# Kernel optimization log

Measured on AMD Instinct MI355X. Metric: run time of the kernel, lower is better.

Reference implementation:

```python
import jax, jax.numpy as jnp
import numpy as np

N_NODES = 50000
N_EDGES = 1_600_000
N_GRAPHS = 64
EMB = 1280
GCN_DIMS = [128, 256, 256]
FC_DIMS = [1024, 128]
EPS = 1e-5  # BatchNorm eps (torch default)


def setup_inputs() -> dict:
    key = jax.random.key(0)
    ks = jax.random.split(key, 16)
    inp = {}
    inp["x"] = jax.random.normal(ks[0], (N_NODES, EMB), jnp.float32)
    inp["edge_index"] = jax.random.randint(ks[1], (2, N_EDGES), 0, N_NODES)
    inp["batch"] = jnp.sort(jax.random.randint(ks[2], (N_NODES,), 0, N_GRAPHS))
    dims = [EMB] + GCN_DIMS
    for i in range(3):
        inp[f"Wg{i}"] = jax.random.normal(ks[3 + i], (dims[i], dims[i + 1]), jnp.float32) * (1.0 / np.sqrt(dims[i]))
        inp[f"bg{i}"] = jnp.zeros((dims[i + 1],), jnp.float32)
        inp[f"gamma{i}"] = jnp.ones((dims[i + 1],), jnp.float32)
        inp[f"beta{i}"] = jnp.zeros((dims[i + 1],), jnp.float32)
    fdims = [GCN_DIMS[-1]] + FC_DIMS
    for i in range(2):
        inp[f"Wf{i}"] = jax.random.normal(ks[10 + i], (fdims[i], fdims[i + 1]), jnp.float32) * (1.0 / np.sqrt(fdims[i]))
        inp[f"bf{i}"] = jnp.zeros((fdims[i + 1],), jnp.float32)
    return inp


def _batchnorm(h, gamma, beta):
    # training-mode BN over node dim, biased variance (torch normalization)
    m = h.mean(axis=0)
    v = h.var(axis=0)
    return gamma * (h - m) * jax.lax.rsqrt(v + EPS) + beta


def reference(x, edge_index, batch,
              Wg0, bg0, gamma0, beta0,
              Wg1, bg1, gamma1, beta1,
              Wg2, bg2, gamma2, beta2,
              Wf0, bf0, Wf1, bf1):
    # --- GCN symmetric normalization with self-loops (PyG GCNConv default) ---
    loop = jnp.arange(N_NODES)
    src = jnp.concatenate([edge_index[0], loop])  # message sources
    dst = jnp.concatenate([edge_index[1], loop])  # aggregation targets
    deg = jax.ops.segment_sum(jnp.ones(src.shape[0], jnp.float32), dst, num_segments=N_NODES)
    dinv = jnp.where(deg > 0, jax.lax.rsqrt(jnp.maximum(deg, 1.0)), 0.0)
    norm = dinv[src] * dinv[dst]  # [E + N]

    def gcn_conv(h, W, b):
        h = h @ W                               # [N, d_out] transform first (PyG order)
        msg = h[src] * norm[:, None]            # gather + scale
        return jax.ops.segment_sum(msg, dst, num_segments=N_NODES) + b

    h = x
    for W, b, g, bt in ((Wg0, bg0, gamma0, beta0),
                        (Wg1, bg1, gamma1, beta1),
                        (Wg2, bg2, gamma2, beta2)):
        h = gcn_conv(h, W, b)
        h = _batchnorm(h, g, bt)
        h = jax.nn.relu(h)
        # dropout is identity in eval mode

    # --- global mean pool over graphs ---
    counts = jax.ops.segment_sum(jnp.ones(N_NODES, jnp.float32), batch, num_segments=N_GRAPHS)
    sums = jax.ops.segment_sum(h, batch, num_segments=N_GRAPHS)
    g = sums / jnp.maximum(counts, 1.0)[:, None]  # [B, 256]

    # --- FC head ---
    g = jax.nn.relu(g @ Wf0 + bf0)
    out = g @ Wf1 + bf1                           # [B, 128]
    return out
```

## Files before the change

kernel.cpp:

```cpp
#include <hip/hip_runtime.h>
#include <hip/hip_bf16.h>

#define N_NODES 50000
#define N_EDGES 1600000
#define N_GRAPHS 64
#define MT_TILES 1563

typedef _Float16 f16;
typedef _Float16 f16x8 __attribute__((ext_vector_type(8)));
typedef _Float16 f16x4 __attribute__((ext_vector_type(4)));
typedef _Float16 f16x2 __attribute__((ext_vector_type(2)));
typedef float f32x4 __attribute__((ext_vector_type(4)));

template <int V> struct VecT;
template <> struct VecT<2> { using type = f16x2; };
template <> struct VecT<4> { using type = f16x4; };

__global__ void init_deg(int* deg) {
    int i = blockIdx.x * blockDim.x + threadIdx.x;
    if (i < N_NODES) deg[i] = 1;
}

__global__ void deg_count(const int* __restrict__ dst, int* __restrict__ deg) {
    int e = blockIdx.x * blockDim.x + threadIdx.x;
    if (e < N_EDGES) atomicAdd(&deg[dst[e]], 1);
}

__global__ void make_dinv(const int* __restrict__ deg, float* __restrict__ dinv) {
    int i = blockIdx.x * blockDim.x + threadIdx.x;
    if (i < N_NODES) dinv[i] = rsqrtf((float)deg[i]);
}

__global__ void scan_deg(const int* __restrict__ deg, int* __restrict__ rowstart,
                         int* __restrict__ pos) {
    __shared__ int wsum[16];
    __shared__ int carry_s;
    const int t = threadIdx.x;
    const int lane = t & 63;
    const int w = t >> 6;
    if (t == 0) carry_s = 0;
    __syncthreads();
    for (int base = 0; base < N_NODES; base += 1024) {
        int i = base + t;
        int v = (i < N_NODES) ? (deg[i] - 1) : 0;
        int s = v;
#pragma unroll
        for (int off = 1; off < 64; off <<= 1) {
            int n = __shfl_up(s, off, 64);
            if (lane >= off) s += n;
        }
        if (lane == 63) wsum[w] = s;
        __syncthreads();
        if (w == 0) {
            int ws = (lane < 16) ? wsum[lane] : 0;
#pragma unroll
            for (int off = 1; off < 16; off <<= 1) {
                int n = __shfl_up(ws, off, 64);
                if (lane >= off) ws += n;
            }
            if (lane < 16) wsum[lane] = ws;
        }
        __syncthreads();
        int waveoff = (w == 0) ? 0 : wsum[w - 1];
        int carry = carry_s;
        int excl = carry + waveoff + s - v;
        if (i < N_NODES) {
            rowstart[i] = excl;
            pos[i] = excl;
        }
        __syncthreads();
        if (t == 0) carry_s = carry + wsum[15];
        __syncthreads();
    }
    if (t == 0) rowstart[N_NODES] = carry_s;
}

__global__ void csr_fill(const int* __restrict__ src, const int* __restrict__ dst,
                         const float* __restrict__ dinv, int* __restrict__ pos,
                         int2* __restrict__ csr) {
    int e = blockIdx.x * blockDim.x + threadIdx.x;
    if (e >= N_EDGES) return;
    int s = src[e], d = dst[e];
    int slot = atomicAdd(&pos[d], 1);
    csr[slot] = make_int2(s, __float_as_int(dinv[s] * dinv[d]));
}

__global__ void cast_w(const float* __restrict__ W, f16* __restrict__ Wt, int K, int N) {
    int i = blockIdx.x * blockDim.x + threadIdx.x;
    if (i >= K * N) return;
    int k = i % K, n = i / K;
    Wt[i] = (f16)W[(size_t)k * N + n];
}

__launch_bounds__(256)
__global__ void cast_x_blocked(const float* __restrict__ x, f16* __restrict__ xb) {
    const int mt = blockIdx.x;
    const int t = threadIdx.x;
    const size_t base = (size_t)mt * 32 * 1280;
    const size_t tbase = (size_t)mt * 40 * 1024;
#pragma unroll 4
    for (int i = 0; i < 40; ++i) {
        int f = i * 1024 + t * 4;
        int r = f / 1280;
        int k = f - r * 1280;
        float4 v = make_float4(0.f, 0.f, 0.f, 0.f);
        if (mt * 32 + r < N_NODES) v = *(const float4*)(x + base + f);
        int kt = k >> 5, kk = k & 31;
        f16x4 o = {(f16)v.x, (f16)v.y, (f16)v.z, (f16)v.w};
        *(f16x4*)(xb + tbase + (size_t)kt * 1024 + r * 32 + kk) = o;
    }
}

__launch_bounds__(256)
__global__ void gemm_xb_f16_sk(const f16* __restrict__ xb, const f16* __restrict__ Bt,
                               float* __restrict__ C0, float* __restrict__ C1) {
    const int K = 1280;
    const int gw = (int)((blockIdx.x * blockDim.x + threadIdx.x) >> 6);
    if (gw >= 6250) return;
    const int lane = threadIdx.x & 63;
    const int m16 = gw >> 1, s = gw & 1;
    const int mt = m16 >> 1, half = m16 & 1;
    float* __restrict__ C = s ? C1 : C0;
    const int r = lane & 15, q = lane >> 4;
    const f16* at = xb + (size_t)mt * 40960 + (size_t)s * 20480 + half * 512 + r * 32 + q * 8;
    const f16* bp = Bt + (size_t)r * K + s * 640 + q * 8;

    f32x4 acc[8];
#pragma unroll
    for (int j = 0; j < 8; ++j) acc[j] = (f32x4){0.f, 0.f, 0.f, 0.f};

#pragma unroll 4
    for (int kt = 0; kt < 20; ++kt) {
        f16x8 a = *(const f16x8*)(at + kt * 1024);
#pragma unroll
        for (int ni = 0; ni < 8; ++ni) {
            f16x8 bf = *(const f16x8*)(bp + (size_t)ni * 16 * K + kt * 32);
            acc[ni] = __builtin_amdgcn_mfma_f32_16x16x32_f16(a, bf, acc[ni], 0, 0, 0);
        }
    }
#pragma unroll
    for (int j = 0; j < 4; ++j) {
        int row = m16 * 16 + q * 4 + j;
        float* cp = C + (size_t)row * 128 + r;
#pragma unroll
        for (int ni = 0; ni < 8; ++ni) cp[ni * 16] = acc[ni][j];
    }
}

__global__ void reduce_cast(const float* __restrict__ c0, const float* __restrict__ c1,
                            f16* __restrict__ o, int n4) {
    int i = blockIdx.x * blockDim.x + threadIdx.x;
    if (i >= n4) return;
    float4 a = ((const float4*)c0)[i];
    float4 b = ((const float4*)c1)[i];
    f16x4 r = {(f16)(a.x + b.x), (f16)(a.y + b.y), (f16)(a.z + b.z), (f16)(a.w + b.w)};
    ((f16x4*)o)[i] = r;
}

template <int K>
__launch_bounds__(256)
__global__ void gemm_h_bn_f16(const f16* __restrict__ A16, const float* __restrict__ ss,
                              const f16* __restrict__ Bt, f16* __restrict__ C16, int N) {
    const int gw = (int)((blockIdx.x * blockDim.x + threadIdx.x) >> 6);
    if (gw >= N_NODES / 16) return;
    const int lane = threadIdx.x & 63;
    const int m0 = gw * 16;
    const int col0 = blockIdx.y * 128;
    const int r = lane & 15, q = lane >> 4;
    const f16* a0 = A16 + (size_t)(m0 + r) * K + q * 8;
    const f16* bp = Bt + (size_t)(col0 + r) * K + q * 8;

    f32x4 acc[8];
#pragma unroll
    for (int j = 0; j < 8; ++j) acc[j] = (f32x4){0.f, 0.f, 0.f, 0.f};

#pragma unroll
    for (int k0 = 0; k0 < K; k0 += 32) {
        f16x8 raw = *(const f16x8*)(a0 + k0);
        const int kb = k0 + q * 8;
        f16x8 af;
#pragma unroll
        for (int j = 0; j < 8; ++j) {
            float v = (float)raw[j] * ss[kb + j] + ss[K + kb + j];
            af[j] = (f16)(v > 0.f ? v : 0.f);
        }
#pragma unroll
        for (int ni = 0; ni < 8; ++ni) {
            f16x8 bf = *(const f16x8*)(bp + (size_t)ni * 16 * K + k0);
            acc[ni] = __builtin_amdgcn_mfma_f32_16x16x32_f16(af, bf, acc[ni], 0, 0, 0);
        }
    }
#pragma unroll
    for (int j = 0; j < 4; ++j) {
        int row = m0 + q * 4 + j;
        f16* cp = C16 + (size_t)row * N + col0 + r;
#pragma unroll
        for (int ni = 0; ni < 8; ++ni) cp[ni * 16] = (f16)acc[ni][j];
    }
}

template <int D>
__launch_bounds__(256)
__global__ void aggregate(const f16* __restrict__ h, const int* __restrict__ rowstart,
                          const int2* __restrict__ csr, const float* __restrict__ dinv,
                          const float* __restrict__ bias, f16* __restrict__ out) {
    constexpr int V = D / 64;
    using vec = typename VecT<V>::type;
    int w = (int)((blockIdx.x * blockDim.x + threadIdx.x) >> 6);
    int lane = threadIdx.x & 63;
    if (w >= N_NODES) return;
    float acc[V];
    float di = dinv[w];
    vec self = *(const vec*)(h + (size_t)w * D + lane * V);
#pragma unroll
    for (int v = 0; v < V; ++v) acc[v] = (float)self[v] * (di * di);
    int e0 = rowstart[w], e1 = rowstart[w + 1];
    int j = e0;
    for (; j + 8 <= e1; j += 8) {
        int2 c[8];
        vec rr[8];
#pragma unroll
        for (int u = 0; u < 8; ++u) c[u] = csr[j + u];
#pragma unroll
        for (int u = 0; u < 8; ++u)
            rr[u] = *(const vec*)(h + (size_t)c[u].x * D + lane * V);
#pragma unroll
        for (int u = 0; u < 8; ++u) {
            float nm = __int_as_float(c[u].y);
#pragma unroll
            for (int v = 0; v < V; ++v) acc[v] += (float)rr[u][v] * nm;
        }
    }
    if (j + 4 <= e1) {
        int2 c0 = csr[j], c1 = csr[j + 1], c2 = csr[j + 2], c3 = csr[j + 3];
        vec r0 = *(const vec*)(h + (size_t)c0.x * D + lane * V);
        vec r1 = *(const vec*)(h + (size_t)c1.x * D + lane * V);
        vec r2 = *(const vec*)(h + (size_t)c2.x * D + lane * V);
        vec r3 = *(const vec*)(h + (size_t)c3.x * D + lane * V);
        float n0 = __int_as_float(c0.y), n1 = __int_as_float(c1.y);
        float n2 = __int_as_float(c2.y), n3 = __int_as_float(c3.y);
#pragma unroll
        for (int v = 0; v < V; ++v)
            acc[v] += (float)r0[v] * n0 + (float)r1[v] * n1 +
                      (float)r2[v] * n2 + (float)r3[v] * n3;
        j += 4;
    }
    for (; j < e1; ++j) {
        int2 c = csr[j];
        vec r = *(const vec*)(h + (size_t)c.x * D + lane * V);
        float nm = __int_as_float(c.y);
#pragma unroll
        for (int v = 0; v < V; ++v) acc[v] += (float)r[v] * nm;
    }
    vec o;
#pragma unroll
    for (int v = 0; v < V; ++v) o[v] = (f16)(acc[v] + bias[lane * V + v]);
    *(vec*)(out + (size_t)w * D + lane * V) = o;
}

template <int D>
__global__ void bn_stats(const f16* __restrict__ h, float* __restrict__ stat) {
    int f = threadIdx.x;
    int r0 = blockIdx.x * 128;
    int r1 = min(r0 + 128, N_NODES);
    float s = 0.f, s2 = 0.f;
    for (int r = r0; r < r1; ++r) {
        float v = (float)h[(size_t)r * D + f];
        s += v;
        s2 += v * v;
    }
    atomicAdd(&stat[f], s);
    atomicAdd(&stat[D + f], s2);
}

template <int D>
__global__ void bn_finalize(const float* __restrict__ stat, const float* __restrict__ gamma,
                            const float* __restrict__ beta, float* __restrict__ ss) {
    int f = threadIdx.x;
    float m = stat[f] * (1.0f / N_NODES);
    float var = stat[D + f] * (1.0f / N_NODES) - m * m;
    float sc = gamma[f] * rsqrtf(var + 1e-5f);
    ss[f] = sc;
    ss[D + f] = beta[f] - m * sc;
}

__global__ void count_batch_bs(const int* __restrict__ batch, int* __restrict__ cnt) {
    int g = threadIdx.x;
    if (g >= N_GRAPHS) return;
    int lo = 0, hi = N_NODES;
    while (lo < hi) { int mid = (lo + hi) >> 1; if (batch[mid] < g) lo = mid + 1; else hi = mid; }
    int b0 = lo;
    lo = 0; hi = N_NODES;
    while (lo < hi) { int mid = (lo + hi) >> 1; if (batch[mid] < g + 1) lo = mid + 1; else hi = mid; }
    cnt[g] = lo - b0;
}

__global__ void pool_seg_bn(const f16* __restrict__ h, const float* __restrict__ ss,
                            const int* __restrict__ batch, float* __restrict__ psum) {
    int f = threadIdx.x;
    float sc = ss[f], sh = ss[256 + f];
    int r0 = blockIdx.x * 64;
    int r1 = min(r0 + 64, N_NODES);
    float acc = 0.f;
    int cur = batch[r0];
    for (int r = r0; r < r1; ++r) {
        int b = batch[r];
        if (b != cur) {
            atomicAdd(&psum[cur * 256 + f], acc);
            acc = 0.f;
            cur = b;
        }
        float v = sc * (float)h[(size_t)r * 256 + f] + sh;
        acc += v > 0.f ? v : 0.f;
    }
    atomicAdd(&psum[cur * 256 + f], acc);
}

__global__ void pool_div(const float* __restrict__ psum, const int* __restrict__ cnt,
                         float* __restrict__ g) {
    int i = blockIdx.x * 256 + threadIdx.x;
    int b = i >> 8;
    float c = (float)max(cnt[b], 1);
    g[i] = psum[i] / c;
}

__global__ void fc_init(const float* __restrict__ b, float* __restrict__ Y, int rows, int N) {
    int i = blockIdx.x * blockDim.x + threadIdx.x;
    if (i < rows * N) Y[i] = b[i % N];
}

__global__ void fc_splitk(const float* __restrict__ X, const float* __restrict__ W,
                          float* __restrict__ Y, int K, int N, int KC) {
    int col = blockIdx.x * blockDim.x + threadIdx.x;
    int row = blockIdx.y;
    int k0 = blockIdx.z * KC;
    float acc = 0.f;
    const float* x = X + (size_t)row * K + k0;
    const float* w = W + (size_t)k0 * N + col;
#pragma unroll 8
    for (int k = 0; k < KC; ++k) acc += x[k] * w[(size_t)k * N];
    atomicAdd(&Y[(size_t)row * N + col], acc);
}

__global__ void relu_inplace(float* __restrict__ Y, int n) {
    int i = blockIdx.x * blockDim.x + threadIdx.x;
    if (i < n) Y[i] = Y[i] > 0.f ? Y[i] : 0.f;
}

extern "C" void kernel_launch(void* const* d_in, const int* in_sizes, int n_in,
                              void* d_out, int out_size, void* d_ws, size_t ws_size,
                              hipStream_t stream) {
    const float* x     = (const float*)d_in[0];
    const int*   ei    = (const int*)d_in[1];
    const int*   batch = (const int*)d_in[2];
    const float* Wg0 = (const float*)d_in[3],  *bg0 = (const float*)d_in[4];
    const float* gamma0 = (const float*)d_in[5], *beta0 = (const float*)d_in[6];
    const float* Wg1 = (const float*)d_in[7],  *bg1 = (const float*)d_in[8];
    const float* gamma1 = (const float*)d_in[9], *beta1 = (const float*)d_in[10];
    const float* Wg2 = (const float*)d_in[11], *bg2 = (const float*)d_in[12];
    const float* gamma2 = (const float*)d_in[13], *beta2 = (const float*)d_in[14];
    const float* Wf0 = (const float*)d_in[15], *bf0 = (const float*)d_in[16];
    const float* Wf1 = (const float*)d_in[17], *bf1 = (const float*)d_in[18];
    float* out = (float*)d_out;

    size_t off = 0;
    auto alloc = [&](size_t bytes) {
        void* p = (char*)d_ws + off;
        off += (bytes + 255) & ~(size_t)255;
        return p;
    };
    f16*   hA16     = (f16*)alloc((size_t)N_NODES * 256 * 2);
    float* cp32     = (float*)alloc((size_t)2 * N_NODES * 128 * 4);
    f16*   hBn16    = (f16*)cp32;
    float* cp0      = cp32;
    float* cp1      = cp32 + (size_t)N_NODES * 128;
    f16*   xb       = (f16*)alloc((size_t)MT_TILES * 40 * 1024 * 2);
    int2*  csr      = (int2*)alloc((size_t)N_EDGES * 8);
    int*   deg      = (int*)alloc((size_t)N_NODES * 4);
    float* dinv     = (float*)alloc((size_t)N_NODES * 4);
    int*   rowstart = (int*)alloc((size_t)(N_NODES + 1) * 4);
    int*   pos      = (int*)alloc((size_t)N_NODES * 4);
    float* bnstat   = (float*)alloc(2 * 256 * 4);
    float* bnss     = (float*)alloc(2 * 256 * 4);
    float* psum     = (float*)alloc(64 * 256 * 4);
    int*   pcount   = (int*)alloc(64 * 4);
    float* gpool    = (float*)alloc(64 * 256 * 4);
    float* g1       = (float*)alloc(64 * 1024 * 4);
    f16*   W0t      = (f16*)alloc((size_t)1280 * 128 * 2);
    f16*   W1t      = (f16*)alloc((size_t)128 * 256 * 2);
    f16*   W2t      = (f16*)alloc((size_t)256 * 256 * 2);
    (void)ws_size;

    const int TPB = 256;
    const int nb_nodes = (N_NODES + TPB - 1) / TPB;
    const int nb_edges = (N_EDGES + TPB - 1) / TPB;

    cast_x_blocked<<<MT_TILES, TPB, 0, stream>>>(x, xb);
    init_deg<<<nb_nodes, TPB, 0, stream>>>(deg);
    deg_count<<<nb_edges, TPB, 0, stream>>>(ei + N_EDGES, deg);
    make_dinv<<<nb_nodes, TPB, 0, stream>>>(deg, dinv);
    scan_deg<<<1, 1024, 0, stream>>>(deg, rowstart, pos);
    csr_fill<<<nb_edges, TPB, 0, stream>>>(ei, ei + N_EDGES, dinv, pos, csr);
    cast_w<<<(1280 * 128 + 255) / 256, 256, 0, stream>>>(Wg0, W0t, 1280, 128);
    cast_w<<<(128 * 256 + 255) / 256, 256, 0, stream>>>(Wg1, W1t, 128, 256);
    cast_w<<<(256 * 256 + 255) / 256, 256, 0, stream>>>(Wg2, W2t, 256, 256);

    const int gemm0_blocks = (6250 * 64 + TPB - 1) / TPB;
    const int gemmh_blocks = (N_NODES / 16 * 64 + TPB - 1) / TPB;
    const int agg_blocks = (N_NODES * 64 + TPB - 1) / TPB;

    gemm_xb_f16_sk<<<gemm0_blocks, TPB, 0, stream>>>(xb, W0t, cp0, cp1);
    reduce_cast<<<(N_NODES * 128 / 4 + 255) / 256, 256, 0, stream>>>(cp0, cp1, hA16, N_NODES * 128 / 4);
    aggregate<128><<<agg_blocks, TPB, 0, stream>>>(hA16, rowstart, csr, dinv, bg0, hBn16);
    hipMemsetAsync(bnstat, 0, 2 * 128 * 4, stream);
    bn_stats<128><<<(N_NODES + 127) / 128, 128, 0, stream>>>(hBn16, bnstat);
    bn_finalize<128><<<1, 128, 0, stream>>>(bnstat, gamma0, beta0, bnss);

    gemm_h_bn_f16<128><<<dim3(gemmh_blocks, 2), TPB, 0, stream>>>(hBn16, bnss, W1t, hA16, 256);
    aggregate<256><<<agg_blocks, TPB, 0, stream>>>(hA16, rowstart, csr, dinv, bg1, hBn16);
    hipMemsetAsync(bnstat, 0, 2 * 256 * 4, stream);
    bn_stats<256><<<(N_NODES + 127) / 128, 256, 0, stream>>>(hBn16, bnstat);
    bn_finalize<256><<<1, 256, 0, stream>>>(bnstat, gamma1, beta1, bnss);

    gemm_h_bn_f16<256><<<dim3(gemmh_blocks, 2), TPB, 0, stream>>>(hBn16, bnss, W2t, hA16, 256);
    aggregate<256><<<agg_blocks, TPB, 0, stream>>>(hA16, rowstart, csr, dinv, bg2, hBn16);
    hipMemsetAsync(bnstat, 0, 2 * 256 * 4, stream);
    bn_stats<256><<<(N_NODES + 127) / 128, 256, 0, stream>>>(hBn16, bnstat);
    bn_finalize<256><<<1, 256, 0, stream>>>(bnstat, gamma2, beta2, bnss);

    hipMemsetAsync(psum, 0, 64 * 256 * 4, stream);
    count_batch_bs<<<1, 64, 0, stream>>>(batch, pcount);
    pool_seg_bn<<<(N_NODES + 63) / 64, 256, 0, stream>>>(hBn16, bnss, batch, psum);
    pool_div<<<64, 256, 0, stream>>>(psum, pcount, gpool);

    fc_init<<<(64 * 1024 + 255) / 256, 256, 0, stream>>>(bf0, g1, 64, 1024);
    fc_splitk<<<dim3(4, 64, 4), 256, 0, stream>>>(gpool, Wf0, g1, 256, 1024, 64);
    relu_inplace<<<(64 * 1024 + 255) / 256, 256, 0, stream>>>(g1, 64 * 1024);
    fc_init<<<(64 * 128 + 255) / 256, 256, 0, stream>>>(bf1, out, 64, 128);
    fc_splitk<<<dim3(1, 64, 16), 128, 0, stream>>>(g1, Wf1, out, 1024, 128, 64);
}
```

Baseline: 1.003 ms.

## Fuse fp32-to-f16 cast into first GEMM and double-buffer GEMM register loads

Drops the separate cast_x_blocked pass and its blocked f16 copy of x. The first GEMM now reads fp32 x directly and converts to f16 in registers. Both GEMM kernels now compute 32 rows per wave, which halves the weight loads per row, and prefetch the next k-slice of A, B and the BN scale/shift into a second register buffer so loads overlap the MFMAs. This saves one full read and write of the 50000x1280 input but raises register pressure and reads A with row-strided uncoalesced fp32 loads.

```diff
diff --git a/kernel.cpp b/kernel.cpp
--- a/kernel.cpp
+++ b/kernel.cpp
@@ -4,7 +4,6 @@
 #define N_NODES 50000
 #define N_EDGES 1600000
 #define N_GRAPHS 64
-#define MT_TILES 1563
 
 typedef _Float16 f16;
 typedef _Float16 f16x8 __attribute__((ext_vector_type(8)));
@@ -93,58 +92,72 @@
 }
 
 __launch_bounds__(256)
-__global__ void cast_x_blocked(const float* __restrict__ x, f16* __restrict__ xb) {
-    const int mt = blockIdx.x;
-    const int t = threadIdx.x;
-    const size_t base = (size_t)mt * 32 * 1280;
-    const size_t tbase = (size_t)mt * 40 * 1024;
-#pragma unroll 4
-    for (int i = 0; i < 40; ++i) {
-        int f = i * 1024 + t * 4;
-        int r = f / 1280;
-        int k = f - r * 1280;
-        float4 v = make_float4(0.f, 0.f, 0.f, 0.f);
-        if (mt * 32 + r < N_NODES) v = *(const float4*)(x + base + f);
-        int kt = k >> 5, kk = k & 31;
-        f16x4 o = {(f16)v.x, (f16)v.y, (f16)v.z, (f16)v.w};
-        *(f16x4*)(xb + tbase + (size_t)kt * 1024 + r * 32 + kk) = o;
-    }
-}
-
-__launch_bounds__(256)
-__global__ void gemm_xb_f16_sk(const f16* __restrict__ xb, const f16* __restrict__ Bt,
-                               float* __restrict__ C0, float* __restrict__ C1) {
-    const int K = 1280;
+__global__ void gemm_x_sk_pipe(const float* __restrict__ A, const f16* __restrict__ Bt,
+                               float* __restrict__ C0, float* __restrict__ C1, int M) {
+    const int K = 1280, KC = 640;
     const int gw = (int)((blockIdx.x * blockDim.x + threadIdx.x) >> 6);
-    if (gw >= 6250) return;
     const int lane = threadIdx.x & 63;
-    const int m16 = gw >> 1, s = gw & 1;
-    const int mt = m16 >> 1, half = m16 & 1;
+    const int tile = gw >> 1, s = gw & 1;
+    const int m0 = tile * 32;
+    if (m0 >= M) return;
     float* __restrict__ C = s ? C1 : C0;
+    const int kbeg = s * KC;
     const int r = lane & 15, q = lane >> 4;
-    const f16* at = xb + (size_t)mt * 40960 + (size_t)s * 20480 + half * 512 + r * 32 + q * 8;
-    const f16* bp = Bt + (size_t)r * K + s * 640 + q * 8;
-
-    f32x4 acc[8];
-#pragma unroll
-    for (int j = 0; j < 8; ++j) acc[j] = (f32x4){0.f, 0.f, 0.f, 0.f};
-
-#pragma unroll 4
+    int row0 = m0 + r;       row0 = row0 < M ? row0 : M - 1;
+    int row1 = m0 + 16 + r;  row1 = row1 < M ? row1 : M - 1;
+    const float* a0 = A + (size_t)row0 * K + kbeg + q * 8;
+    const float* a1 = A + (size_t)row1 * K + kbeg + q * 8;
+    const f16* bp = Bt + (size_t)r * K + kbeg + q * 8;
+
+    f32x4 acc[2][8];
+#pragma unroll
+    for (int i = 0; i < 2; ++i)
+#pragma unroll
+        for (int j = 0; j < 8; ++j) acc[i][j] = (f32x4){0.f, 0.f, 0.f, 0.f};
+
+    float4 ab[2][4];
+    f16x8 bb[2][8];
+    ab[0][0] = *(const float4*)(a0);
+    ab[0][1] = *(const float4*)(a0 + 4);
+    ab[0][2] = *(const float4*)(a1);
+    ab[0][3] = *(const float4*)(a1 + 4);
+#pragma unroll
+    for (int ni = 0; ni < 8; ++ni) bb[0][ni] = *(const f16x8*)(bp + (size_t)ni * 16 * K);
+
+#pragma unroll
     for (int kt = 0; kt < 20; ++kt) {
-        f16x8 a = *(const f16x8*)(at + kt * 1024);
+        const int cur = kt & 1, nxt = cur ^ 1;
+        if (kt < 19) {
+            const int ko = (kt + 1) * 32;
+            ab[nxt][0] = *(const float4*)(a0 + ko);
+            ab[nxt][1] = *(const float4*)(a0 + ko + 4);
+            ab[nxt][2] = *(const float4*)(a1 + ko);
+            ab[nxt][3] = *(const float4*)(a1 + ko + 4);
+#pragma unroll
+            for (int ni = 0; ni < 8; ++ni)
+                bb[nxt][ni] = *(const f16x8*)(bp + (size_t)ni * 16 * K + ko);
+        }
+        f16x8 af0 = {(f16)ab[cur][0].x, (f16)ab[cur][0].y, (f16)ab[cur][0].z, (f16)ab[cur][0].w,
+                     (f16)ab[cur][1].x, (f16)ab[cur][1].y, (f16)ab[cur][1].z, (f16)ab[cur][1].w};
+        f16x8 af1 = {(f16)ab[cur][2].x, (f16)ab[cur][2].y, (f16)ab[cur][2].z, (f16)ab[cur][2].w,
+                     (f16)ab[cur][3].x, (f16)ab[cur][3].y, (f16)ab[cur][3].z, (f16)ab[cur][3].w};
 #pragma unroll
         for (int ni = 0; ni < 8; ++ni) {
-            f16x8 bf = *(const f16x8*)(bp + (size_t)ni * 16 * K + kt * 32);
-            acc[ni] = __builtin_amdgcn_mfma_f32_16x16x32_f16(a, bf, acc[ni], 0, 0, 0);
-        }
-    }
-#pragma unroll
-    for (int j = 0; j < 4; ++j) {
-        int row = m16 * 16 + q * 4 + j;
-        float* cp = C + (size_t)row * 128 + r;
-#pragma unroll
-        for (int ni = 0; ni < 8; ++ni) cp[ni * 16] = acc[ni][j];
-    }
+            acc[0][ni] = __builtin_amdgcn_mfma_f32_16x16x32_f16(af0, bb[cur][ni], acc[0][ni], 0, 0, 0);
+            acc[1][ni] = __builtin_amdgcn_mfma_f32_16x16x32_f16(af1, bb[cur][ni], acc[1][ni], 0, 0, 0);
+        }
+    }
+#pragma unroll
+    for (int mi = 0; mi < 2; ++mi)
+#pragma unroll
+        for (int j = 0; j < 4; ++j) {
+            int row = m0 + mi * 16 + q * 4 + j;
+            if (row < M) {
+                float* cp = C + (size_t)row * 128 + r;
+#pragma unroll
+                for (int ni = 0; ni < 8; ++ni) cp[ni * 16] = acc[mi][ni][j];
+            }
+        }
 }
 
 __global__ void reduce_cast(const float* __restrict__ c0, const float* __restrict__ c1,
@@ -159,44 +172,85 @@
 
 template <int K>
 __launch_bounds__(256)
-__global__ void gemm_h_bn_f16(const f16* __restrict__ A16, const float* __restrict__ ss,
-                              const f16* __restrict__ Bt, f16* __restrict__ C16, int N) {
+__global__ void gemm_h_bn_pipe(const f16* __restrict__ A16, const float* __restrict__ ss,
+                               const f16* __restrict__ Bt, f16* __restrict__ C16, int N) {
+    constexpr int NT = K / 32;
     const int gw = (int)((blockIdx.x * blockDim.x + threadIdx.x) >> 6);
-    if (gw >= N_NODES / 16) return;
     const int lane = threadIdx.x & 63;
-    const int m0 = gw * 16;
+    const int m0 = gw * 32;
+    if (m0 >= N_NODES) return;
     const int col0 = blockIdx.y * 128;
     const int r = lane & 15, q = lane >> 4;
-    const f16* a0 = A16 + (size_t)(m0 + r) * K + q * 8;
+    int row0 = m0 + r;       row0 = row0 < N_NODES ? row0 : N_NODES - 1;
+    int row1 = m0 + 16 + r;  row1 = row1 < N_NODES ? row1 : N_NODES - 1;
+    const f16* a0 = A16 + (size_t)row0 * K + q * 8;
+    const f16* a1 = A16 + (size_t)row1 * K + q * 8;
     const f16* bp = Bt + (size_t)(col0 + r) * K + q * 8;
-
-    f32x4 acc[8];
-#pragma unroll
-    for (int j = 0; j < 8; ++j) acc[j] = (f32x4){0.f, 0.f, 0.f, 0.f};
-
-#pragma unroll
-    for (int k0 = 0; k0 < K; k0 += 32) {
-        f16x8 raw = *(const f16x8*)(a0 + k0);
-        const int kb = k0 + q * 8;
-        f16x8 af;
+    const float* scp = ss + q * 8;
+    const float* shp = ss + K + q * 8;
+
+    f32x4 acc[2][8];
+#pragma unroll
+    for (int i = 0; i < 2; ++i)
+#pragma unroll
+        for (int j = 0; j < 8; ++j) acc[i][j] = (f32x4){0.f, 0.f, 0.f, 0.f};
+
+    f16x8 ab[2][2];
+    f16x8 bb[2][8];
+    float4 sb[2][4];
+    ab[0][0] = *(const f16x8*)(a0);
+    ab[0][1] = *(const f16x8*)(a1);
+    sb[0][0] = *(const float4*)(scp);
+    sb[0][1] = *(const float4*)(scp + 4);
+    sb[0][2] = *(const float4*)(shp);
+    sb[0][3] = *(const float4*)(shp + 4);
+#pragma unroll
+    for (int ni = 0; ni < 8; ++ni) bb[0][ni] = *(const f16x8*)(bp + (size_t)ni * 16 * K);
+
+#pragma unroll
+    for (int kt = 0; kt < NT; ++kt) {
+        const int cur = kt & 1, nxt = cur ^ 1;
+        if (kt < NT - 1) {
+            const int ko = (kt + 1) * 32;
+            ab[nxt][0] = *(const f16x8*)(a0 + ko);
+            ab[nxt][1] = *(const f16x8*)(a1 + ko);
+            sb[nxt][0] = *(const float4*)(scp + ko);
+            sb[nxt][1] = *(const float4*)(scp + ko + 4);
+            sb[nxt][2] = *(const float4*)(shp + ko);
+            sb[nxt][3] = *(const float4*)(shp + ko + 4);
+#pragma unroll
+            for (int ni = 0; ni < 8; ++ni)
+                bb[nxt][ni] = *(const f16x8*)(bp + (size_t)ni * 16 * K + ko);
+        }
+        float sc[8] = {sb[cur][0].x, sb[cur][0].y, sb[cur][0].z, sb[cur][0].w,
+                       sb[cur][1].x, sb[cur][1].y, sb[cur][1].z, sb[cur][1].w};
+        float sh[8] = {sb[cur][2].x, sb[cur][2].y, sb[cur][2].z, sb[cur][2].w,
+                       sb[cur][3].x, sb[cur][3].y, sb[cur][3].z, sb[cur][3].w};
+        f16x8 af0, af1;
 #pragma unroll
         for (int j = 0; j < 8; ++j) {
-            float v = (float)raw[j] * ss[kb + j] + ss[K + kb + j];
-            af[j] = (f16)(v > 0.f ? v : 0.f);
+            float v0 = (float)ab[cur][0][j] * sc[j] + sh[j];
+            float v1 = (float)ab[cur][1][j] * sc[j] + sh[j];
+            af0[j] = (f16)(v0 > 0.f ? v0 : 0.f);
+            af1[j] = (f16)(v1 > 0.f ? v1 : 0.f);
         }
 #pragma unroll
         for (int ni = 0; ni < 8; ++ni) {
-            f16x8 bf = *(const f16x8*)(bp + (size_t)ni * 16 * K + k0);
-            acc[ni] = __builtin_amdgcn_mfma_f32_16x16x32_f16(af, bf, acc[ni], 0, 0, 0);
-        }
-    }
-#pragma unroll
-    for (int j = 0; j < 4; ++j) {
-        int row = m0 + q * 4 + j;
-        f16* cp = C16 + (size_t)row * N + col0 + r;
-#pragma unroll
-        for (int ni = 0; ni < 8; ++ni) cp[ni * 16] = (f16)acc[ni][j];
-    }
+            acc[0][ni] = __builtin_amdgcn_mfma_f32_16x16x32_f16(af0, bb[cur][ni], acc[0][ni], 0, 0, 0);
+            acc[1][ni] = __builtin_amdgcn_mfma_f32_16x16x32_f16(af1, bb[cur][ni], acc[1][ni], 0, 0, 0);
+        }
+    }
+#pragma unroll
+    for (int mi = 0; mi < 2; ++mi)
+#pragma unroll
+        for (int j = 0; j < 4; ++j) {
+            int row = m0 + mi * 16 + q * 4 + j;
+            if (row < N_NODES) {
+                f16* cp = C16 + (size_t)row * N + col0 + r;
+#pragma unroll
+                for (int ni = 0; ni < 8; ++ni) cp[ni * 16] = (f16)acc[mi][ni][j];
+            }
+        }
 }
 
 template <int D>
@@ -374,7 +428,6 @@
     f16*   hBn16    = (f16*)cp32;
     float* cp0      = cp32;
     float* cp1      = cp32 + (size_t)N_NODES * 128;
-    f16*   xb       = (f16*)alloc((size_t)MT_TILES * 40 * 1024 * 2);
     int2*  csr      = (int2*)alloc((size_t)N_EDGES * 8);
     int*   deg      = (int*)alloc((size_t)N_NODES * 4);
     float* dinv     = (float*)alloc((size_t)N_NODES * 4);
@@ -395,7 +448,6 @@
     const int nb_nodes = (N_NODES + TPB - 1) / TPB;
     const int nb_edges = (N_EDGES + TPB - 1) / TPB;
 
-    cast_x_blocked<<<MT_TILES, TPB, 0, stream>>>(x, xb);
     init_deg<<<nb_nodes, TPB, 0, stream>>>(deg);
     deg_count<<<nb_edges, TPB, 0, stream>>>(ei + N_EDGES, deg);
     make_dinv<<<nb_nodes, TPB, 0, stream>>>(deg, dinv);
@@ -405,24 +457,24 @@
     cast_w<<<(128 * 256 + 255) / 256, 256, 0, stream>>>(Wg1, W1t, 128, 256);
     cast_w<<<(256 * 256 + 255) / 256, 256, 0, stream>>>(Wg2, W2t, 256, 256);
 
-    const int gemm0_blocks = (6250 * 64 + TPB - 1) / TPB;
-    const int gemmh_blocks = (N_NODES / 16 * 64 + TPB - 1) / TPB;
+    const int gemm0_blocks = (1563 * 2 * 64 + TPB - 1) / TPB;
+    const int gemmh_blocks = (1563 * 64 + TPB - 1) / TPB;
     const int agg_blocks = (N_NODES * 64 + TPB - 1) / TPB;
 
-    gemm_xb_f16_sk<<<gemm0_blocks, TPB, 0, stream>>>(xb, W0t, cp0, cp1);
+    gemm_x_sk_pipe<<<gemm0_blocks, TPB, 0, stream>>>(x, W0t, cp0, cp1, N_NODES);
     reduce_cast<<<(N_NODES * 128 / 4 + 255) / 256, 256, 0, stream>>>(cp0, cp1, hA16, N_NODES * 128 / 4);
     aggregate<128><<<agg_blocks, TPB, 0, stream>>>(hA16, rowstart, csr, dinv, bg0, hBn16);
     hipMemsetAsync(bnstat, 0, 2 * 128 * 4, stream);
     bn_stats<128><<<(N_NODES + 127) / 128, 128, 0, stream>>>(hBn16, bnstat);
     bn_finalize<128><<<1, 128, 0, stream>>>(bnstat, gamma0, beta0, bnss);
 
-    gemm_h_bn_f16<128><<<dim3(gemmh_blocks, 2), TPB, 0, stream>>>(hBn16, bnss, W1t, hA16, 256);
+    gemm_h_bn_pipe<128><<<dim3(gemmh_blocks, 2), TPB, 0, stream>>>(hBn16, bnss, W1t, hA16, 256);
     aggregate<256><<<agg_blocks, TPB, 0, stream>>>(hA16, rowstart, csr, dinv, bg1, hBn16);
     hipMemsetAsync(bnstat, 0, 2 * 256 * 4, stream);
     bn_stats<256><<<(N_NODES + 127) / 128, 256, 0, stream>>>(hBn16, bnstat);
     bn_finalize<256><<<1, 256, 0, stream>>>(bnstat, gamma1, beta1, bnss);
 
-    gemm_h_bn_f16<256><<<dim3(gemmh_blocks, 2), TPB, 0, stream>>>(hBn16, bnss, W2t, hA16, 256);
+    gemm_h_bn_pipe<256><<<dim3(gemmh_blocks, 2), TPB, 0, stream>>>(hBn16, bnss, W2t, hA16, 256);
     aggregate<256><<<agg_blocks, TPB, 0, stream>>>(hA16, rowstart, csr, dinv, bg2, hBn16);
     hipMemsetAsync(bnstat, 0, 2 * 256 * 4, stream);
     bn_stats<256><<<(N_NODES + 127) / 128, 256, 0, stream>>>(hBn16, bnstat);
```

New measurement: 895.3 us. 10.7% less time.
